# Optimization experiments

Hardware: AMD Instinct MI355X
Metric: run time of the kernel (lower is better)

## Reference

```python
import jax, jax.numpy as jnp
import numpy as np

EPS = 1e-5

def lrelu(x):
    return jnp.where(x >= 0, x, 0.1 * x)

def bn_eval(x, g, b, m, v):
    # eval-mode BatchNorm over the last (channel) axis
    return (x - m) * (g * jax.lax.rsqrt(v + EPS)) + b

def setup_inputs():
    key = jax.random.key(0)
    ks = jax.random.split(key, 12)
    Nq, K, Cin, Fc, Co = 20000, 32, 3, 64, 64
    q_points = jax.random.normal(ks[0], (Nq, Cin), jnp.float32)
    s_points = jax.random.normal(ks[1], (Nq, Cin), jnp.float32)
    feat = jax.random.normal(ks[2], (Nq, Fc), jnp.float32)
    # valid indices 0..Nq (Nq == shadow/pad row appended in forward)
    neighb_inds = jax.random.randint(ks[3], (Nq, K), 0, Nq + 1)
    def w(k, shape, fan_in):
        return jax.random.normal(k, shape, jnp.float32) / np.float32(np.sqrt(fan_in))
    W_pos2 = w(ks[4], (Fc, Cin), Cin)          # convpos2: Conv2d(Cin, Fc, 1)
    W_attn = w(ks[5], (Co * Cin, Fc), Fc)      # convattn: Conv2d(Fc, Co*Cin, 1)
    W_res = w(ks[6], (Co, Fc), Fc)             # residual 1x1 conv
    def bn(k, c):
        k1, k2, k3, k4 = jax.random.split(k, 4)
        return (jax.random.normal(k1, (c,), jnp.float32) * 0.1 + 1.0,
                jax.random.normal(k2, (c,), jnp.float32) * 0.1,
                jax.random.normal(k3, (c,), jnp.float32) * 0.1,
                jax.random.uniform(k4, (c,), jnp.float32) * 0.5 + 0.5)
    bq = bn(ks[7], Fc); bp = bn(ks[8], Cin); b1 = bn(ks[9], Co); br = bn(ks[10], Co)
    return dict(q_points=q_points, s_points=s_points, neighb_inds=neighb_inds, feat=feat,
                W_pos2=W_pos2, W_attn=W_attn, W_res=W_res,
                bnq_g=bq[0], bnq_b=bq[1], bnq_m=bq[2], bnq_v=bq[3],
                bnp_g=bp[0], bnp_b=bp[1], bnp_m=bp[2], bnp_v=bp[3],
                bn1_g=b1[0], bn1_b=b1[1], bn1_m=b1[2], bn1_v=b1[3],
                bnr_g=br[0], bnr_b=br[1], bnr_m=br[2], bnr_v=br[3])

def reference(q_points, s_points, neighb_inds, feat, W_pos2, W_attn, W_res,
              bnq_g, bnq_b, bnq_m, bnq_v, bnp_g, bnp_b, bnp_m, bnp_v,
              bn1_g, bn1_b, bn1_m, bn1_v, bnr_g, bnr_b, bnr_m, bnr_v):
    Nq, Cin = q_points.shape
    Fc = feat.shape[1]
    Co = W_res.shape[0]
    K = neighb_inds.shape[1]
    # append shadow (zero) row for out-of-range neighbor indices
    s_pad = jnp.concatenate([s_points, jnp.zeros((1, Cin), s_points.dtype)], 0)
    f_pad = jnp.concatenate([feat, jnp.zeros((1, Fc), feat.dtype)], 0)
    xg = s_pad[neighb_inds]                      # [Nq,K,Cin] EFR_P gather
    yg = f_pad[neighb_inds]                      # [Nq,K,Fc]  EFR_F gather
    x_v = xg - q_points[:, None, :]              # [Nq,K,Cin] values
    x_q = lrelu(bn_eval(feat, bnq_g, bnq_b, bnq_m, bnq_v))          # [Nq,Fc]
    pos0 = lrelu(bn_eval(s_points, bnp_g, bnp_b, bnp_m, bnp_v))     # [Nq,Cin]
    pos = (pos0[:, None, :] - x_v) @ W_pos2.T                       # [Nq,K,Fc]
    attn = x_q[:, None, :] - yg + pos                               # [Nq,K,Fc]
    attn = jax.nn.softmax(attn / jnp.sqrt(jnp.float32(Fc)), axis=1) # softmax over K
    attn = (attn @ W_attn.T).reshape(Nq, K, Co, Cin)                # [Nq,K,Co,Cin]
    y_e = jnp.einsum('nkoi,nki->nko', attn, x_v)                    # [Nq,K,Co]
    y_e = lrelu(bn_eval(y_e, bn1_g, bn1_b, bn1_m, bn1_v))
    res = bn_eval(yg @ W_res.T, bnr_g, bnr_b, bnr_m, bnr_v)         # [Nq,K,Co]
    y_e = lrelu(y_e + res)
    return y_e.max(axis=1)                                          # [Nq,Co]
```

## Files before the change

### kernel.cpp

```cpp
#include <hip/hip_runtime.h>
#include <math.h>

#define KNB 32
#define FC 64
#define CO 64
#define EPS 1e-5f
#define NBLOCKS 1024

typedef __attribute__((ext_vector_type(8))) short short8;
typedef __attribute__((ext_vector_type(4))) float floatx4;

__device__ __forceinline__ short f2bf(float x) {
    unsigned int u = __float_as_uint(x);
    u += 0x7FFFu + ((u >> 16) & 1u);
    return (short)(u >> 16);
}
__device__ __forceinline__ float bf2f(short s) {
    return __uint_as_float(((unsigned int)(unsigned short)s) << 16);
}
__device__ __forceinline__ float lrelu(float x) { return fmaxf(x, 0.1f * x); }

__global__ __launch_bounds__(256, 4) void GCT_61272003445298_kernel(
    const float* __restrict__ q_points,
    const float* __restrict__ s_points,
    const int*   __restrict__ neighb,
    const float* __restrict__ feat,
    const float* __restrict__ W_pos2,
    const float* __restrict__ W_attn,
    const float* __restrict__ W_res,
    const float* __restrict__ bnq_g, const float* __restrict__ bnq_b,
    const float* __restrict__ bnq_m, const float* __restrict__ bnq_v,
    const float* __restrict__ bnp_g, const float* __restrict__ bnp_b,
    const float* __restrict__ bnp_m, const float* __restrict__ bnp_v,
    const float* __restrict__ bn1_g, const float* __restrict__ bn1_b,
    const float* __restrict__ bn1_m, const float* __restrict__ bn1_v,
    const float* __restrict__ bnr_g, const float* __restrict__ bnr_b,
    const float* __restrict__ bnr_m, const float* __restrict__ bnr_v,
    float* __restrict__ out, int Nq)
{
    const int t = threadIdx.x;
    const int wv = t >> 6;
    const int lane = t & 63;
    const int cc = lane & 15, quad = lane >> 4;
    const int o = wv * 16 + cc;

    __shared__ __align__(16) short sA1[64 * 72];
    __shared__ __align__(16) short sA2[64 * 72];
    __shared__ float sXv[64][4];
    __shared__ float sXq[2][64];
    __shared__ float sPos0[2][4];
    __shared__ float sWp[192];
    __shared__ float sQs[64], sQb[64];
    __shared__ float sPs[4], sPb[4];
    __shared__ int   sIdx[64];

    if (t < 192) sWp[t] = W_pos2[t];
    if (t < 64) {
        float sc = bnq_g[t] * rsqrtf(bnq_v[t] + EPS);
        sQs[t] = sc; sQb[t] = bnq_b[t] - bnq_m[t] * sc;
        if (t < 3) {
            float scp = bnp_g[t] * rsqrtf(bnp_v[t] + EPS);
            sPs[t] = scp; sPb[t] = bnp_b[t] - bnp_m[t] * scp;
        }
    }
    const float e1s = bn1_g[o] * rsqrtf(bn1_v[o] + EPS);
    const float e1b = bn1_b[o] - bn1_m[o] * e1s;
    const float ers = bnr_g[o] * rsqrtf(bnr_v[o] + EPS);
    const float erb = bnr_b[o] - bnr_m[o] * ers;

    short8 bW[4][2];
    #pragma unroll
    for (int ty = 0; ty < 4; ++ty) {
        const float* wrow = (ty < 3) ? (W_attn + (long)(o * 3 + ty) * FC)
                                     : (W_res  + (long)o * FC);
        #pragma unroll
        for (int ks = 0; ks < 2; ++ks) {
            int k0 = ks * 32 + quad * 8;
            float4 w0 = *(const float4*)(wrow + k0);
            float4 w1 = *(const float4*)(wrow + k0 + 4);
            short8 b;
            b[0] = f2bf(w0.x); b[1] = f2bf(w0.y); b[2] = f2bf(w0.z); b[3] = f2bf(w0.w);
            b[4] = f2bf(w1.x); b[5] = f2bf(w1.y); b[6] = f2bf(w1.z); b[7] = f2bf(w1.w);
            bW[ty][ks] = b;
        }
    }
    __syncthreads();

    const int npair = (Nq + 1) >> 1;
    for (int p = blockIdx.x; p < npair; p += NBLOCKS) {
        const long n0 = 2L * p;
        long n1 = n0 + 1;
        const bool has1 = (n1 < Nq);
        if (!has1) n1 = n0;

        if (t < 64) {
            int q = t >> 5;
            long nn = q ? n1 : n0;
            int idx = neighb[nn * KNB + (t & 31)];
            sIdx[t] = idx;
            float q0 = q_points[nn * 3 + 0];
            float q1v = q_points[nn * 3 + 1];
            float q2 = q_points[nn * 3 + 2];
            float x0 = 0.f, x1 = 0.f, x2 = 0.f;
            if (idx < Nq) {
                x0 = s_points[(long)idx * 3 + 0];
                x1 = s_points[(long)idx * 3 + 1];
                x2 = s_points[(long)idx * 3 + 2];
            }
            sXv[t][0] = x0 - q0; sXv[t][1] = x1 - q1v; sXv[t][2] = x2 - q2;
            if (t < 6) {
                int qq = t / 3, i = t % 3;
                long nn2 = qq ? n1 : n0;
                sPos0[qq][i] = lrelu(s_points[nn2 * 3 + i] * sPs[i] + sPb[i]);
            }
        } else if (t >= 192) {
            int f = t - 192;
            float sc = sQs[f], bb = sQb[f];
            sXq[0][f] = lrelu(feat[n0 * FC + f] * sc + bb);
            sXq[1][f] = lrelu(feat[n1 * FC + f] * sc + bb);
        }
        __syncthreads();

        #pragma unroll
        for (int it = 0; it < 4; ++it) {
            int e = it * 256 + t;
            int row = e >> 4, fq = e & 15;
            int q = row >> 5;
            int idx = sIdx[row];
            float4 y;
            if (idx < Nq) y = *(const float4*)(feat + (long)idx * FC + fq * 4);
            else          y = make_float4(0.f, 0.f, 0.f, 0.f);
            *(short4*)(sA2 + row * 72 + fq * 4) =
                make_short4(f2bf(y.x), f2bf(y.y), f2bf(y.z), f2bf(y.w));
            float d0 = sPos0[q][0] - sXv[row][0];
            float d1 = sPos0[q][1] - sXv[row][1];
            float d2 = sPos0[q][2] - sXv[row][2];
            float4 xq4 = *(const float4*)&sXq[q][fq * 4];
            float yv[4]  = {y.x, y.y, y.z, y.w};
            float xqv[4] = {xq4.x, xq4.y, xq4.z, xq4.w};
            short lb[4];
            #pragma unroll
            for (int c = 0; c < 4; ++c) {
                int f = fq * 4 + c;
                float pos = sWp[f * 3 + 0] * d0 + sWp[f * 3 + 1] * d1 + sWp[f * 3 + 2] * d2;
                lb[c] = f2bf((xqv[c] - yv[c] + pos) * 0.125f);
            }
            *(short4*)(sA1 + row * 72 + fq * 4) = make_short4(lb[0], lb[1], lb[2], lb[3]);
        }
        __syncthreads();

        {
            int col = t >> 1, h = t & 1;
            int q = col >> 6, f = col & 63;
            short* pp = sA1 + (q * 32 + h * 16) * 72 + f;
            float l[16];
            float m = -1e30f;
            #pragma unroll
            for (int j = 0; j < 16; ++j) { l[j] = bf2f(pp[j * 72]); m = fmaxf(m, l[j]); }
            m = fmaxf(m, __shfl_xor(m, 1));
            float s = 0.f;
            #pragma unroll
            for (int j = 0; j < 16; ++j) { float e = __expf(l[j] - m); s += e; l[j] = e; }
            s += __shfl_xor(s, 1);
            float inv = 1.f / s;
            #pragma unroll
            for (int j = 0; j < 16; ++j) pp[j * 72] = f2bf(l[j] * inv);
        }
        __syncthreads();

        float m0 = -1e30f, m1 = -1e30f;
        #pragma unroll
        for (int mt = 0; mt < 4; ++mt) {
            floatx4 acc[4];
            #pragma unroll
            for (int ty = 0; ty < 4; ++ty) acc[ty] = (floatx4){0.f, 0.f, 0.f, 0.f};
            int r0 = mt * 16 + cc;
            #pragma unroll
            for (int ks = 0; ks < 2; ++ks) {
                int kof = ks * 32 + quad * 8;
                short8 a1 = *(const short8*)(sA1 + r0 * 72 + kof);
                short8 a2 = *(const short8*)(sA2 + r0 * 72 + kof);
                acc[0] = __builtin_amdgcn_mfma_f32_16x16x32_bf16(a1, bW[0][ks], acc[0], 0, 0, 0);
                acc[1] = __builtin_amdgcn_mfma_f32_16x16x32_bf16(a1, bW[1][ks], acc[1], 0, 0, 0);
                acc[2] = __builtin_amdgcn_mfma_f32_16x16x32_bf16(a1, bW[2][ks], acc[2], 0, 0, 0);
                acc[3] = __builtin_amdgcn_mfma_f32_16x16x32_bf16(a2, bW[3][ks], acc[3], 0, 0, 0);
            }
            #pragma unroll
            for (int reg = 0; reg < 4; ++reg) {
                int r = mt * 16 + quad * 4 + reg;
                float4 xv = *(const float4*)&sXv[r][0];
                float y = acc[0][reg] * xv.x + acc[1][reg] * xv.y + acc[2][reg] * xv.z;
                float ybn = lrelu(y * e1s + e1b);
                float rbn = acc[3][reg] * ers + erb;
                float v = lrelu(ybn + rbn);
                if (mt < 2) m0 = fmaxf(m0, v); else m1 = fmaxf(m1, v);
            }
        }
        m0 = fmaxf(m0, __shfl_xor(m0, 16));
        m0 = fmaxf(m0, __shfl_xor(m0, 32));
        m1 = fmaxf(m1, __shfl_xor(m1, 16));
        m1 = fmaxf(m1, __shfl_xor(m1, 32));
        if (lane < 16) {
            out[n0 * CO + o] = m0;
            if (has1) out[n1 * CO + o] = m1;
        }
        __syncthreads();
    }
}

extern "C" void kernel_launch(void* const* d_in, const int* in_sizes, int n_in,
                              void* d_out, int out_size, void* d_ws, size_t ws_size,
                              hipStream_t stream) {
    const float* q_points = (const float*)d_in[0];
    const float* s_points = (const float*)d_in[1];
    const int*   neighb   = (const int*)  d_in[2];
    const float* feat     = (const float*)d_in[3];
    const float* W_pos2   = (const float*)d_in[4];
    const float* W_attn   = (const float*)d_in[5];
    const float* W_res    = (const float*)d_in[6];
    const float* bnq_g = (const float*)d_in[7];
    const float* bnq_b = (const float*)d_in[8];
    const float* bnq_m = (const float*)d_in[9];
    const float* bnq_v = (const float*)d_in[10];
    const float* bnp_g = (const float*)d_in[11];
    const float* bnp_b = (const float*)d_in[12];
    const float* bnp_m = (const float*)d_in[13];
    const float* bnp_v = (const float*)d_in[14];
    const float* bn1_g = (const float*)d_in[15];
    const float* bn1_b = (const float*)d_in[16];
    const float* bn1_m = (const float*)d_in[17];
    const float* bn1_v = (const float*)d_in[18];
    const float* bnr_g = (const float*)d_in[19];
    const float* bnr_b = (const float*)d_in[20];
    const float* bnr_m = (const float*)d_in[21];
    const float* bnr_v = (const float*)d_in[22];
    float* out = (float*)d_out;

    int Nq = in_sizes[0] / 3;

    hipLaunchKernelGGL(GCT_61272003445298_kernel,
                       dim3(NBLOCKS), dim3(256), 0, stream,
                       q_points, s_points, neighb, feat, W_pos2, W_attn, W_res,
                       bnq_g, bnq_b, bnq_m, bnq_v,
                       bnp_g, bnp_b, bnp_m, bnp_v,
                       bn1_g, bn1_b, bn1_m, bn1_v,
                       bnr_g, bnr_b, bnr_m, bnr_v,
                       out, Nq);
}
```

Measured before the change: 173.2 us.

## Fold per-query position term into logit bias and simplify softmax stage

Folds the per-query position contribution (pos0 @ W_pos2) and the 1/sqrt(Fc) scale into a per-query constant vector. The per-neighbor logit is now a few FMAs using per-thread register copies of pre-scaled W_pos2. Adds packed bf16 conversion with simple round-half-up and drops the max subtraction in the softmax. The softmax is remapped to process two features per thread, with reductions done by shuffles across quads. Also raises the block count and occupancy hint. Skipping the max subtraction risks overflow if logits grow large.

```diff
diff --git a/kernel.cpp b/kernel.cpp
--- a/kernel.cpp
+++ b/kernel.cpp
@@ -5,22 +5,22 @@
 #define FC 64
 #define CO 64
 #define EPS 1e-5f
-#define NBLOCKS 1024
+#define NBLOCKS 1536
 
 typedef __attribute__((ext_vector_type(8))) short short8;
 typedef __attribute__((ext_vector_type(4))) float floatx4;
 
+__device__ __forceinline__ unsigned int pkbf(float a, float b) {
+    unsigned int ua = (__float_as_uint(a) + 0x8000u) >> 16;
+    unsigned int ub = (__float_as_uint(b) + 0x8000u) & 0xFFFF0000u;
+    return ua | ub;
+}
 __device__ __forceinline__ short f2bf(float x) {
-    unsigned int u = __float_as_uint(x);
-    u += 0x7FFFu + ((u >> 16) & 1u);
-    return (short)(u >> 16);
-}
-__device__ __forceinline__ float bf2f(short s) {
-    return __uint_as_float(((unsigned int)(unsigned short)s) << 16);
+    return (short)((__float_as_uint(x) + 0x8000u) >> 16);
 }
 __device__ __forceinline__ float lrelu(float x) { return fmaxf(x, 0.1f * x); }
 
-__global__ __launch_bounds__(256, 4) void GCT_61272003445298_kernel(
+__global__ __launch_bounds__(256, 6) void GCT_61272003445298_kernel(
     const float* __restrict__ q_points,
     const float* __restrict__ s_points,
     const int*   __restrict__ neighb,
@@ -47,14 +47,13 @@
     __shared__ __align__(16) short sA1[64 * 72];
     __shared__ __align__(16) short sA2[64 * 72];
     __shared__ float sXv[64][4];
-    __shared__ float sXq[2][64];
-    __shared__ float sPos0[2][4];
-    __shared__ float sWp[192];
+    __shared__ __align__(16) float sXqc[2][64];
+    __shared__ __align__(16) float sWp2[192];
     __shared__ float sQs[64], sQb[64];
     __shared__ float sPs[4], sPb[4];
     __shared__ int   sIdx[64];
 
-    if (t < 192) sWp[t] = W_pos2[t];
+    if (t < 192) sWp2[t] = 0.125f * W_pos2[t];
     if (t < 64) {
         float sc = bnq_g[t] * rsqrtf(bnq_v[t] + EPS);
         sQs[t] = sc; sQb[t] = bnq_b[t] - bnq_m[t] * sc;
@@ -86,6 +85,12 @@
     }
     __syncthreads();
 
+    const int fq = t & 15, rbase = t >> 4;
+    float wp[12];
+    *(float4*)&wp[0] = *(const float4*)&sWp2[fq * 12];
+    *(float4*)&wp[4] = *(const float4*)&sWp2[fq * 12 + 4];
+    *(float4*)&wp[8] = *(const float4*)&sWp2[fq * 12 + 8];
+
     const int npair = (Nq + 1) >> 1;
     for (int p = blockIdx.x; p < npair; p += NBLOCKS) {
         const long n0 = 2L * p;
@@ -108,63 +113,71 @@
                 x2 = s_points[(long)idx * 3 + 2];
             }
             sXv[t][0] = x0 - q0; sXv[t][1] = x1 - q1v; sXv[t][2] = x2 - q2;
-            if (t < 6) {
-                int qq = t / 3, i = t % 3;
-                long nn2 = qq ? n1 : n0;
-                sPos0[qq][i] = lrelu(s_points[nn2 * 3 + i] * sPs[i] + sPb[i]);
-            }
         } else if (t >= 192) {
             int f = t - 192;
-            float sc = sQs[f], bb = sQb[f];
-            sXq[0][f] = lrelu(feat[n0 * FC + f] * sc + bb);
-            sXq[1][f] = lrelu(feat[n1 * FC + f] * sc + bb);
-        }
-        __syncthreads();
-
-        #pragma unroll
-        for (int it = 0; it < 4; ++it) {
-            int e = it * 256 + t;
-            int row = e >> 4, fq = e & 15;
-            int q = row >> 5;
-            int idx = sIdx[row];
-            float4 y;
-            if (idx < Nq) y = *(const float4*)(feat + (long)idx * FC + fq * 4);
-            else          y = make_float4(0.f, 0.f, 0.f, 0.f);
-            *(short4*)(sA2 + row * 72 + fq * 4) =
-                make_short4(f2bf(y.x), f2bf(y.y), f2bf(y.z), f2bf(y.w));
-            float d0 = sPos0[q][0] - sXv[row][0];
-            float d1 = sPos0[q][1] - sXv[row][1];
-            float d2 = sPos0[q][2] - sXv[row][2];
-            float4 xq4 = *(const float4*)&sXq[q][fq * 4];
-            float yv[4]  = {y.x, y.y, y.z, y.w};
-            float xqv[4] = {xq4.x, xq4.y, xq4.z, xq4.w};
-            short lb[4];
-            #pragma unroll
-            for (int c = 0; c < 4; ++c) {
-                int f = fq * 4 + c;
-                float pos = sWp[f * 3 + 0] * d0 + sWp[f * 3 + 1] * d1 + sWp[f * 3 + 2] * d2;
-                lb[c] = f2bf((xqv[c] - yv[c] + pos) * 0.125f);
-            }
-            *(short4*)(sA1 + row * 72 + fq * 4) = make_short4(lb[0], lb[1], lb[2], lb[3]);
+            float xq0 = lrelu(fmaf(feat[n0 * FC + f], sQs[f], sQb[f]));
+            float xq1 = lrelu(fmaf(feat[n1 * FC + f], sQs[f], sQb[f]));
+            float c0 = 0.125f * xq0, c1 = 0.125f * xq1;
+            #pragma unroll
+            for (int i = 0; i < 3; ++i) {
+                float p0 = lrelu(fmaf(s_points[n0 * 3 + i], sPs[i], sPb[i]));
+                float p1 = lrelu(fmaf(s_points[n1 * 3 + i], sPs[i], sPb[i]));
+                float w = sWp2[f * 3 + i];
+                c0 = fmaf(p0, w, c0);
+                c1 = fmaf(p1, w, c1);
+            }
+            sXqc[0][f] = c0; sXqc[1][f] = c1;
         }
         __syncthreads();
 
         {
-            int col = t >> 1, h = t & 1;
-            int q = col >> 6, f = col & 63;
-            short* pp = sA1 + (q * 32 + h * 16) * 72 + f;
-            float l[16];
-            float m = -1e30f;
-            #pragma unroll
-            for (int j = 0; j < 16; ++j) { l[j] = bf2f(pp[j * 72]); m = fmaxf(m, l[j]); }
-            m = fmaxf(m, __shfl_xor(m, 1));
-            float s = 0.f;
-            #pragma unroll
-            for (int j = 0; j < 16; ++j) { float e = __expf(l[j] - m); s += e; l[j] = e; }
-            s += __shfl_xor(s, 1);
-            float inv = 1.f / s;
-            #pragma unroll
-            for (int j = 0; j < 16; ++j) pp[j * 72] = f2bf(l[j] * inv);
+            float4 xqc0 = *(const float4*)&sXqc[0][fq * 4];
+            float4 xqc1 = *(const float4*)&sXqc[1][fq * 4];
+            #pragma unroll
+            for (int it = 0; it < 4; ++it) {
+                int row = it * 16 + rbase;
+                float4 xqc = (it < 2) ? xqc0 : xqc1;
+                int idx = sIdx[row];
+                float4 y = make_float4(0.f, 0.f, 0.f, 0.f);
+                if (idx < Nq) y = *(const float4*)(feat + (long)idx * FC + fq * 4);
+                uint2 pk; pk.x = pkbf(y.x, y.y); pk.y = pkbf(y.z, y.w);
+                *(uint2*)(sA2 + row * 72 + fq * 4) = pk;
+                float4 xv = *(const float4*)&sXv[row][0];
+                float l0 = fmaf(y.x, -0.125f, xqc.x);
+                l0 = fmaf(-xv.x, wp[0], l0); l0 = fmaf(-xv.y, wp[1], l0); l0 = fmaf(-xv.z, wp[2], l0);
+                float l1 = fmaf(y.y, -0.125f, xqc.y);
+                l1 = fmaf(-xv.x, wp[3], l1); l1 = fmaf(-xv.y, wp[4], l1); l1 = fmaf(-xv.z, wp[5], l1);
+                float l2 = fmaf(y.z, -0.125f, xqc.z);
+                l2 = fmaf(-xv.x, wp[6], l2); l2 = fmaf(-xv.y, wp[7], l2); l2 = fmaf(-xv.z, wp[8], l2);
+                float l3 = fmaf(y.w, -0.125f, xqc.w);
+                l3 = fmaf(-xv.x, wp[9], l3); l3 = fmaf(-xv.y, wp[10], l3); l3 = fmaf(-xv.z, wp[11], l3);
+                uint2 pl; pl.x = pkbf(l0, l1); pl.y = pkbf(l2, l3);
+                *(uint2*)(sA1 + row * 72 + fq * 4) = pl;
+            }
+        }
+        __syncthreads();
+
+        {
+            const int q = wv >> 1;
+            const int f2 = ((wv & 1) << 4) + cc;
+            const int row0 = q * 32 + quad * 8;
+            short* base = sA1 + row0 * 72 + f2 * 2;
+            float elo[8], ehi[8];
+            float slo = 0.f, shi = 0.f;
+            #pragma unroll
+            for (int j = 0; j < 8; ++j) {
+                unsigned u = *(const unsigned*)(base + j * 72);
+                float flo = __uint_as_float(u << 16);
+                float fhi = __uint_as_float(u & 0xFFFF0000u);
+                elo[j] = __expf(flo); ehi[j] = __expf(fhi);
+                slo += elo[j]; shi += ehi[j];
+            }
+            slo += __shfl_xor(slo, 16); slo += __shfl_xor(slo, 32);
+            shi += __shfl_xor(shi, 16); shi += __shfl_xor(shi, 32);
+            float ilo = 1.f / slo, ihi = 1.f / shi;
+            #pragma unroll
+            for (int j = 0; j < 8; ++j)
+                *(unsigned*)(base + j * 72) = pkbf(elo[j] * ilo, ehi[j] * ihi);
         }
         __syncthreads();
 
```

After: 248.5 us. +43.5%, slower.
